# Optimization experiments

Hardware: AMD Instinct MI355X
Metric: run time of the kernel (lower is better)

Reference implementation:

```python
import jax, jax.numpy as jnp
import numpy as np

N, E, F, H, O, B = 100000, 1200000, 64, 1024, 1, 256


def _gcn_conv(x, W, b, src, dst, ew, num_nodes):
    # PyG GCNConv: out_i = sum_{(s->i)} d_i^{-1/2} w_e d_s^{-1/2} (x_s W) + b
    deg = jax.ops.segment_sum(ew, dst, num_segments=num_nodes)
    dinv = jnp.where(deg > 0, jax.lax.rsqrt(jnp.maximum(deg, 1e-12)), 0.0)
    norm = dinv[src] * ew * dinv[dst]          # [E]
    h = x @ W                                   # [N, out]
    msg = h[src] * norm[:, None]                # gather + scale
    return jax.ops.segment_sum(msg, dst, num_segments=num_nodes) + b


def setup_inputs() -> dict:
    key = jax.random.key(0)
    ks = jax.random.split(key, 12)
    def lin(k, fan_in, fan_out):
        s = 1.0 / np.sqrt(fan_in)
        kw, kb = jax.random.split(k)
        return (jax.random.uniform(kw, (fan_in, fan_out), jnp.float32, -s, s),
                jax.random.uniform(kb, (fan_out,), jnp.float32, -s, s))
    W1, b1 = lin(ks[0], F, F)
    W2, b2 = lin(ks[1], F, 2 * F)
    W3, b3 = lin(ks[2], 2 * F, 4 * F)
    Wf1, bf1 = lin(ks[3], 5 * F, H)
    Wf2, bf2 = lin(ks[4], H, O)
    feature = jax.random.normal(ks[5], (N, F), jnp.float32)
    edge_index = jax.random.randint(ks[6], (2, E), 0, N, jnp.int32)
    weight = jax.random.uniform(ks[7], (E,), jnp.float32)
    protein_batch = jnp.sort(jax.random.randint(ks[8], (N,), 0, B, jnp.int32))
    return {"feature": feature, "edge_index": edge_index, "weight": weight,
            "protein_batch": protein_batch,
            "W1": W1, "b1": b1, "W2": W2, "b2": b2, "W3": W3, "b3": b3,
            "Wf1": Wf1, "bf1": bf1, "Wf2": Wf2, "bf2": bf2}


def reference(feature, edge_index, weight, protein_batch,
              W1, b1, W2, b2, W3, b3, Wf1, bf1, Wf2, bf2):
    num_nodes = feature.shape[0]
    # add self-loops with weight 1 (PyG default)
    loop = jnp.arange(num_nodes, dtype=edge_index.dtype)
    src = jnp.concatenate([edge_index[0], loop])
    dst = jnp.concatenate([edge_index[1], loop])
    ew = jnp.concatenate([weight, jnp.ones((num_nodes,), weight.dtype)])

    x = jax.nn.relu(_gcn_conv(feature, W1, b1, src, dst, ew, num_nodes))
    x = jax.nn.relu(_gcn_conv(x, W2, b2, src, dst, ew, num_nodes))
    x = jax.nn.relu(_gcn_conv(x, W3, b3, src, dst, ew, num_nodes))
    x = jnp.concatenate([x, feature], axis=1)   # [N, 5F]

    # global_mean_pool over graph ids
    sums = jax.ops.segment_sum(x, protein_batch, num_segments=B)
    cnts = jax.ops.segment_sum(jnp.ones((num_nodes,), x.dtype), protein_batch, num_segments=B)
    gc = sums / jnp.maximum(cnts, 1.0)[:, None]

    gc = jax.nn.relu(gc @ Wf1 + bf1)            # dropout is identity in eval
    return gc @ Wf2 + bf2
```

## Files before the change

kernel.cpp:

```cpp
#include <hip/hip_runtime.h>
#include <cstdio>
#include <cstdint>

typedef _Float16 f16x8 __attribute__((ext_vector_type(8)));
typedef float f32x4 __attribute__((ext_vector_type(4)));

__device__ inline unsigned short f2bf(float f) {
  unsigned u = __float_as_uint(f);
  u += 0x7fffu + ((u >> 16) & 1u);
  return (unsigned short)(u >> 16);
}
__device__ inline float bf2f(unsigned short h) {
  return __uint_as_float(((unsigned)h) << 16);
}
__device__ inline unsigned short f2h(float f) {
  union { _Float16 h; unsigned short u; } cv;
  cv.h = (_Float16)f;
  return cv.u;
}


__global__ __launch_bounds__(256)
void k_prep(float* __restrict__ psum,
            const float* __restrict__ feature, ushort* __restrict__ featb,
            const float* __restrict__ W1, ushort* __restrict__ w1h,
            const float* __restrict__ W2, ushort* __restrict__ w2h,
            const float* __restrict__ W3, ushort* __restrict__ w3h,
            int BC, int NF, int F, int D2, int D3,
            int nB, int nC) {
  int b = blockIdx.x;
  int t = threadIdx.x;
  if (b < nB) {
    int i = b * 256 + t;
    if (i < BC) psum[i] = 0.f;
  } else if (b < nB + nC) {
    int base = ((b - nB) * 256 + t) * 4;
    if (base < NF) {
      float4 v = *reinterpret_cast<const float4*>(feature + base);
      ushort4 h;
      h.x = f2bf(v.x); h.y = f2bf(v.y); h.z = f2bf(v.z); h.w = f2bf(v.w);
      *reinterpret_cast<ushort4*>(featb + base) = h;
    }
  } else {
    int idx = (b - nB - nC) * 256 + t;
    int s1 = F * F, s2 = s1 + F * D2, s3 = s2 + D2 * D3;
    if (idx < s1) {
      int k = idx / F, n = idx - k * F;
      w1h[(size_t)n * F + k] = f2h(W1[idx]);
    } else if (idx < s2) {
      int i2 = idx - s1; int k = i2 / D2, n = i2 - k * D2;
      w2h[(size_t)n * F + k] = f2h(W2[i2]);
    } else if (idx < s3) {
      int i3 = idx - s2; int k = i3 / D3, n = i3 - k * D3;
      w3h[(size_t)n * D2 + k] = f2h(W3[i3]);
    }
  }
}

__global__ __launch_bounds__(256)
void k_gbound(const int* __restrict__ pb, int* __restrict__ gs, int N, int B) {
  int b = blockIdx.x * 256 + threadIdx.x;
  if (b > B) return;
  int lo = 0, hi = N;
  while (lo < hi) {
    int mid = (lo + hi) >> 1;
    if (pb[mid] < b) lo = mid + 1; else hi = mid;
  }
  gs[b] = lo;
}


#define EPB 4096

__global__ __launch_bounds__(256)
void k_bhist(const int* __restrict__ dst, int* __restrict__ H,
             int NB, int E) {
  __shared__ int hist[512];
  const int t = threadIdx.x;
  for (int i = t; i < NB; i += 256) hist[i] = 0;
  __syncthreads();
  const int base = blockIdx.x * EPB + t;
#pragma unroll
  for (int j = 0; j < EPB / 256; j++) {
    int e = base + 256 * j;
    if (e < E) atomicAdd(&hist[dst[e] >> 8], 1);
  }
  __syncthreads();
  for (int i = t; i < NB; i += 256) H[(size_t)blockIdx.x * NB + i] = hist[i];
}

__global__ __launch_bounds__(256)
void k_bscan1(const int* __restrict__ H, int* __restrict__ S,
              int* __restrict__ bsum, int NB, int NBLK, int T) {
  __shared__ int sh[256];
  const int t = threadIdx.x;
  const int base = blockIdx.x * 1024;
  int v[4]; int s = 0;
#pragma unroll
  for (int j = 0; j < 4; j++) {
    int idx = base + t * 4 + j;
    if (idx < T) {
      int bin = idx / NBLK, bi = idx - bin * NBLK;
      v[j] = H[(size_t)bi * NB + bin];
    } else v[j] = 0;
    s += v[j];
  }
  sh[t] = s;
  __syncthreads();
  for (int off = 1; off < 256; off <<= 1) {
    int x = (t >= off) ? sh[t - off] : 0;
    __syncthreads();
    sh[t] += x;
    __syncthreads();
  }
  int run = sh[t] - s;
#pragma unroll
  for (int j = 0; j < 4; j++) {
    int idx = base + t * 4 + j;
    if (idx < T) S[idx] = run;
    run += v[j];
  }
  if (t == 255) bsum[blockIdx.x] = sh[255];
}

__global__ __launch_bounds__(256)
void k_bscan23(int* __restrict__ S, const int* __restrict__ bsum, int T) {
  __shared__ int spre;
  const int chunk = blockIdx.x >> 2;
  if (threadIdx.x == 0) {
    int pre = 0;
    for (int t = 0; t < chunk; t++) pre += bsum[t];
    spre = pre;
  }
  __syncthreads();
  int i = blockIdx.x * 256 + threadIdx.x;
  if (i < T) S[i] += spre;
}

__global__ __launch_bounds__(256)
void k_bscatter(const int* __restrict__ src, const int* __restrict__ dst,
                const float* __restrict__ ew, const int* __restrict__ S,
                int* __restrict__ sdst, int2* __restrict__ ssw,
                int NB, int NBLK, int E) {
  __shared__ int cnt[512];
  __shared__ int sbase[512];
  const int t = threadIdx.x, bi = blockIdx.x;
  for (int i = t; i < NB; i += 256) {
    cnt[i] = 0;
    sbase[i] = S[(size_t)i * NBLK + bi];
  }
  __syncthreads();
  const int base = bi * EPB + t;
#pragma unroll
  for (int j = 0; j < EPB / 256; j++) {
    int e = base + 256 * j;
    if (e < E) {
      int d = dst[e];
      int bin = d >> 8;
      int r = atomicAdd(&cnt[bin], 1);
      int pos = sbase[bin] + r;
      sdst[pos] = d;
      ssw[pos] = make_int2(src[e], __float_as_int(ew[e]));
    }
  }
}

__global__ __launch_bounds__(256)
void k_bprocA(const int* __restrict__ sdst, const int2* __restrict__ ssw,
              const int* __restrict__ S, int* __restrict__ cntN,
              float* __restrict__ wsumN, int NB, int NBLK, int N, int E) {
  __shared__ int cnt[256];
  __shared__ float wsm[256];
  const int t = threadIdx.x, bin = blockIdx.x;
  cnt[t] = 0; wsm[t] = 0.f;
  __syncthreads();
  const int start = S[(size_t)bin * NBLK];
  const int end = (bin + 1 < NB) ? S[(size_t)(bin + 1) * NBLK] : E;
  for (int p = start + t; p < end; p += 256) {
    int ld = sdst[p] & 255;
    atomicAdd(&cnt[ld], 1);
    atomicAdd(&wsm[ld], __int_as_float(ssw[p].y));
  }
  __syncthreads();
  int n = bin * 256 + t;
  if (n < N) { cntN[n] = cnt[t]; wsumN[n] = wsm[t]; }
}

__global__ __launch_bounds__(256)
void k_scan1(const int* __restrict__ cntN, const float* __restrict__ wsumN,
             int* __restrict__ rs, int* __restrict__ bsum,
             float* __restrict__ dinv, float* __restrict__ sn, int N) {
  __shared__ int sh[256];
  const int t = threadIdx.x;
  const int base = blockIdx.x * 1024;
  int v[4]; int s = 0;
#pragma unroll
  for (int j = 0; j < 4; j++) {
    int idx = base + t * 4 + j;
    if (idx < N) {
      v[j] = cntN[idx];
      double deg = 1.0 + (double)wsumN[idx];
      float r = (float)(1.0 / sqrt(deg));
      dinv[idx] = r;
      sn[idx] = r * r;
    } else v[j] = 0;
    s += v[j];
  }
  sh[t] = s;
  __syncthreads();
  for (int off = 1; off < 256; off <<= 1) {
    int x = (t >= off) ? sh[t - off] : 0;
    __syncthreads();
    sh[t] += x;
    __syncthreads();
  }
  int run = sh[t] - s;
#pragma unroll
  for (int j = 0; j < 4; j++) {
    int idx = base + t * 4 + j;
    if (idx < N) rs[idx] = run;
    run += v[j];
  }
  if (t == 255) bsum[blockIdx.x] = sh[255];
}

__global__ __launch_bounds__(256)
void k_scan23(int* __restrict__ rs, const int* __restrict__ bsum, int N, int E) {
  __shared__ int spre;
  const int chunk = blockIdx.x >> 2;
  if (threadIdx.x == 0) {
    int pre = 0;
    for (int t = 0; t < chunk; t++) pre += bsum[t];
    spre = pre;
  }
  __syncthreads();
  int i = blockIdx.x * 256 + threadIdx.x;
  if (i < N) rs[i] += spre;
  if (i == 0) rs[N] = E;
}

__global__ __launch_bounds__(256)
void k_bprocB(const int* __restrict__ sdst, const int2* __restrict__ ssw,
              const int* __restrict__ S, const int* __restrict__ rs,
              const float* __restrict__ dinv,
              int2* __restrict__ epack, int NB, int NBLK, int N, int E) {
  __shared__ int cnt[256];
  __shared__ float sdv[256];
  __shared__ int srs[256];
  const int t = threadIdx.x, bin = blockIdx.x;
  cnt[t] = 0;
  int n = bin * 256 + t;
  sdv[t] = (n < N) ? dinv[n] : 0.f;
  srs[t] = (n < N) ? rs[n] : 0;
  __syncthreads();
  const int start = S[(size_t)bin * NBLK];
  const int end = (bin + 1 < NB) ? S[(size_t)(bin + 1) * NBLK] : E;
  for (int p = start + t; p < end; p += 256) {
    int d = sdst[p];
    int ld = d & 255;
    int2 sw = ssw[p];
    int r = atomicAdd(&cnt[ld], 1);
    float w = dinv[sw.x] * __int_as_float(sw.y) * sdv[ld];
    epack[srs[ld] + r] = make_int2(sw.x, __float_as_int(w));
  }
}


__device__ inline void bf8_fma(const int4 v, float w, float* acc) {
  acc[0] = fmaf(__uint_as_float((unsigned)v.x << 16), w, acc[0]);
  acc[1] = fmaf(__uint_as_float((unsigned)v.x & 0xffff0000u), w, acc[1]);
  acc[2] = fmaf(__uint_as_float((unsigned)v.y << 16), w, acc[2]);
  acc[3] = fmaf(__uint_as_float((unsigned)v.y & 0xffff0000u), w, acc[3]);
  acc[4] = fmaf(__uint_as_float((unsigned)v.z << 16), w, acc[4]);
  acc[5] = fmaf(__uint_as_float((unsigned)v.z & 0xffff0000u), w, acc[5]);
  acc[6] = fmaf(__uint_as_float((unsigned)v.w << 16), w, acc[6]);
  acc[7] = fmaf(__uint_as_float((unsigned)v.w & 0xffff0000u), w, acc[7]);
}

template<int LOG2L>
__global__ __launch_bounds__(256)
void k_aggregate_b(const ushort* __restrict__ Xb, const int* __restrict__ rs,
                   const int2* __restrict__ epack, const float* __restrict__ sn,
                   ushort* __restrict__ AH, int N) {
  const int t = blockIdx.x * blockDim.x + threadIdx.x;
  const int row = t >> LOG2L;
  if (row >= N) return;
  const int L = 1 << LOG2L;
  const int D = L << 3;
  const int c = (t & (L - 1)) << 3;
  const ushort* __restrict__ Xc = Xb + c;

  float acc[8];
  {
    int4 v = *reinterpret_cast<const int4*>(Xc + (size_t)row * D);
    float s = sn[row];
    acc[0] = s * __uint_as_float((unsigned)v.x << 16);
    acc[1] = s * __uint_as_float((unsigned)v.x & 0xffff0000u);
    acc[2] = s * __uint_as_float((unsigned)v.y << 16);
    acc[3] = s * __uint_as_float((unsigned)v.y & 0xffff0000u);
    acc[4] = s * __uint_as_float((unsigned)v.z << 16);
    acc[5] = s * __uint_as_float((unsigned)v.z & 0xffff0000u);
    acc[6] = s * __uint_as_float((unsigned)v.w << 16);
    acc[7] = s * __uint_as_float((unsigned)v.w & 0xffff0000u);
  }
  const int p0 = rs[row], pe = rs[row + 1];
  int i = p0;
  if ((i & 1) && i < pe) {
    int2 e = epack[i];
    int4 v = *reinterpret_cast<const int4*>(Xc + (size_t)e.x * D);
    bf8_fma(v, __int_as_float(e.y), acc);
    i++;
  }
  for (; i + 8 <= pe; i += 8) {
    int4 ea = *reinterpret_cast<const int4*>(&epack[i]);
    int4 eb = *reinterpret_cast<const int4*>(&epack[i + 2]);
    int4 ec = *reinterpret_cast<const int4*>(&epack[i + 4]);
    int4 ed = *reinterpret_cast<const int4*>(&epack[i + 6]);
    int4 v0 = *reinterpret_cast<const int4*>(Xc + (size_t)ea.x * D);
    int4 v1 = *reinterpret_cast<const int4*>(Xc + (size_t)ea.z * D);
    int4 v2 = *reinterpret_cast<const int4*>(Xc + (size_t)eb.x * D);
    int4 v3 = *reinterpret_cast<const int4*>(Xc + (size_t)eb.z * D);
    int4 v4 = *reinterpret_cast<const int4*>(Xc + (size_t)ec.x * D);
    int4 v5 = *reinterpret_cast<const int4*>(Xc + (size_t)ec.z * D);
    int4 v6 = *reinterpret_cast<const int4*>(Xc + (size_t)ed.x * D);
    int4 v7 = *reinterpret_cast<const int4*>(Xc + (size_t)ed.z * D);
    bf8_fma(v0, __int_as_float(ea.y), acc);
    bf8_fma(v1, __int_as_float(ea.w), acc);
    bf8_fma(v2, __int_as_float(eb.y), acc);
    bf8_fma(v3, __int_as_float(eb.w), acc);
    bf8_fma(v4, __int_as_float(ec.y), acc);
    bf8_fma(v5, __int_as_float(ec.w), acc);
    bf8_fma(v6, __int_as_float(ed.y), acc);
    bf8_fma(v7, __int_as_float(ed.w), acc);
  }
  if (i + 4 <= pe) {
    int4 ea = *reinterpret_cast<const int4*>(&epack[i]);
    int4 eb = *reinterpret_cast<const int4*>(&epack[i + 2]);
    int4 v0 = *reinterpret_cast<const int4*>(Xc + (size_t)ea.x * D);
    int4 v1 = *reinterpret_cast<const int4*>(Xc + (size_t)ea.z * D);
    int4 v2 = *reinterpret_cast<const int4*>(Xc + (size_t)eb.x * D);
    int4 v3 = *reinterpret_cast<const int4*>(Xc + (size_t)eb.z * D);
    bf8_fma(v0, __int_as_float(ea.y), acc);
    bf8_fma(v1, __int_as_float(ea.w), acc);
    bf8_fma(v2, __int_as_float(eb.y), acc);
    bf8_fma(v3, __int_as_float(eb.w), acc);
    i += 4;
  }
  if (i + 2 <= pe) {
    int4 e2 = *reinterpret_cast<const int4*>(&epack[i]);
    int4 v0 = *reinterpret_cast<const int4*>(Xc + (size_t)e2.x * D);
    int4 v1 = *reinterpret_cast<const int4*>(Xc + (size_t)e2.z * D);
    bf8_fma(v0, __int_as_float(e2.y), acc);
    bf8_fma(v1, __int_as_float(e2.w), acc);
    i += 2;
  }
  if (i < pe) {
    int2 e = epack[i];
    int4 v = *reinterpret_cast<const int4*>(Xc + (size_t)e.x * D);
    bf8_fma(v, __int_as_float(e.y), acc);
  }
  ushort h[8];
#pragma unroll
  for (int j = 0; j < 8; j++) h[j] = f2h(acc[j]);
  size_t o = (size_t)row * D + c;
  *reinterpret_cast<ushort4*>(AH + o)     = make_ushort4(h[0], h[1], h[2], h[3]);
  *reinterpret_cast<ushort4*>(AH + o + 4) = make_ushort4(h[4], h[5], h[6], h[7]);
}


template<int KT, int NT>
__global__ __launch_bounds__(256)
void k_gemm_mfma(const ushort* __restrict__ Ah, const ushort* __restrict__ Bh,
                 const float* __restrict__ bias, ushort* __restrict__ Y,
                 int N, int D) {
  const int t = threadIdx.x;
  const int wave = t >> 6, lane = t & 63;
  const int quad = lane >> 4, l16 = lane & 15;
  const int m0 = blockIdx.y * 128;
  const int n0 = blockIdx.x * NT;

  int r0 = m0 + wave * 32 + l16;
  int r1 = r0 + 16;
  if (r0 >= N) r0 = N - 1;
  if (r1 >= N) r1 = N - 1;
  const ushort* __restrict__ A0 = Ah + (size_t)r0 * KT;
  const ushort* __restrict__ A1 = Ah + (size_t)r1 * KT;
  const ushort* __restrict__ Bq = Bh + (size_t)(n0 + l16) * KT + quad * 8;

  f32x4 acc[2][NT / 16];
#pragma unroll
  for (int mi = 0; mi < 2; mi++)
#pragma unroll
    for (int ni = 0; ni < NT / 16; ni++) acc[mi][ni] = (f32x4){0.f, 0.f, 0.f, 0.f};

#pragma unroll
  for (int k0 = 0; k0 < KT; k0 += 32) {
    const int kk = k0 + quad * 8;
    f16x8 a0 = *reinterpret_cast<const f16x8*>(A0 + kk);
    f16x8 a1 = *reinterpret_cast<const f16x8*>(A1 + kk);
#pragma unroll
    for (int ni = 0; ni < NT / 16; ni++) {
      f16x8 bH = *reinterpret_cast<const f16x8*>(Bq + (size_t)(ni * 16) * KT + k0);
      acc[0][ni] = __builtin_amdgcn_mfma_f32_16x16x32_f16(a0, bH, acc[0][ni], 0, 0, 0);
      acc[1][ni] = __builtin_amdgcn_mfma_f32_16x16x32_f16(a1, bH, acc[1][ni], 0, 0, 0);
    }
  }

#pragma unroll
  for (int mi = 0; mi < 2; mi++) {
    int rb = m0 + wave * 32 + mi * 16 + quad * 4;
#pragma unroll
    for (int ni = 0; ni < NT / 16; ni++) {
      int col = n0 + ni * 16 + l16;
      float bv = bias[col];
#pragma unroll
      for (int r = 0; r < 4; r++) {
        int row = rb + r;
        if (row < N)
          Y[(size_t)row * D + col] = f2bf(fmaxf(acc[mi][ni][r] + bv, 0.f));
      }
    }
  }
}


#define PSPLIT 4

__global__ void k_pool(const ushort* __restrict__ X3b, const float* __restrict__ feat,
                       const int* __restrict__ gs, float* __restrict__ psum,
                       int D3, int F) {
  const int c = threadIdx.x;
  const int C = D3 + F;
  const int b = blockIdx.y;
  const int sp = blockIdx.x;
  const int s0 = gs[b], e0 = gs[b + 1];
  const int len = e0 - s0;
  if (len <= 0) return;
  const int chunk = (len + PSPLIT - 1) / PSPLIT;
  const int s = s0 + sp * chunk;
  int e = s + chunk; if (e > e0) e = e0;
  if (s >= e) return;
  const int n = e - s;
  float a0 = 0.f, a1 = 0.f, a2 = 0.f, a3 = 0.f;
  float a4 = 0.f, a5 = 0.f, a6 = 0.f, a7 = 0.f;
  if (c < D3) {
    const ushort* p = X3b + (size_t)s * D3 + c;
    int i = 0;
    for (; i + 8 <= n; i += 8) {
      a0 += bf2f(p[0 * (size_t)D3]);
      a1 += bf2f(p[1 * (size_t)D3]);
      a2 += bf2f(p[2 * (size_t)D3]);
      a3 += bf2f(p[3 * (size_t)D3]);
      a4 += bf2f(p[4 * (size_t)D3]);
      a5 += bf2f(p[5 * (size_t)D3]);
      a6 += bf2f(p[6 * (size_t)D3]);
      a7 += bf2f(p[7 * (size_t)D3]);
      p += 8 * (size_t)D3;
    }
    for (; i < n; i++) { a0 += bf2f(*p); p += D3; }
  } else {
    const float* p = feat + (size_t)s * F + (c - D3);
    int i = 0;
    for (; i + 8 <= n; i += 8) {
      a0 += p[0 * (size_t)F];
      a1 += p[1 * (size_t)F];
      a2 += p[2 * (size_t)F];
      a3 += p[3 * (size_t)F];
      a4 += p[4 * (size_t)F];
      a5 += p[5 * (size_t)F];
      a6 += p[6 * (size_t)F];
      a7 += p[7 * (size_t)F];
      p += 8 * (size_t)F;
    }
    for (; i < n; i++) { a0 += *p; p += F; }
  }
  float tot = ((a0 + a1) + (a2 + a3)) + ((a4 + a5) + (a6 + a7));
  atomicAdd(&psum[(size_t)b * C + c], tot);
}


__global__ __launch_bounds__(256)
void k_fc1(const float* __restrict__ psum, const int* __restrict__ gs,
           const float* __restrict__ Wf1, const float* __restrict__ bf1,
           float* __restrict__ hidden, int C, int Hh) {
  const int b = blockIdx.y;
  __shared__ float gcs[384];
  float invc = 1.f / fmaxf((float)(gs[b + 1] - gs[b]), 1.f);
  for (int c = threadIdx.x; c < C; c += 256)
    gcs[c] = psum[(size_t)b * C + c] * invc;
  __syncthreads();
  const int j = blockIdx.x * 256 + threadIdx.x;
  if (j >= Hh) return;
  const float* w = Wf1 + j;
  float a0 = 0.f, a1 = 0.f, a2 = 0.f, a3 = 0.f;
  int c = 0;
  for (; c + 4 <= C; c += 4) {
    a0 = fmaf(gcs[c + 0], w[(size_t)(c + 0) * Hh], a0);
    a1 = fmaf(gcs[c + 1], w[(size_t)(c + 1) * Hh], a1);
    a2 = fmaf(gcs[c + 2], w[(size_t)(c + 2) * Hh], a2);
    a3 = fmaf(gcs[c + 3], w[(size_t)(c + 3) * Hh], a3);
  }
  for (; c < C; c++) a0 = fmaf(gcs[c], w[(size_t)c * Hh], a0);
  float r = ((a0 + a1) + (a2 + a3)) + bf1[j];
  hidden[(size_t)b * Hh + j] = fmaxf(r, 0.f);
}

__global__ void k_fc2(const float* __restrict__ hidden, const float* __restrict__ Wf2,
                      const float* __restrict__ bf2, float* __restrict__ out, int Hh) {
  int b = blockIdx.x;
  int lane = threadIdx.x;
  double s = 0.0;
  for (int j = lane; j < Hh; j += 64) s += (double)hidden[(size_t)b * Hh + j] * (double)Wf2[j];
#pragma unroll
  for (int off = 32; off > 0; off >>= 1) s += __shfl_down(s, off);
  if (lane == 0) out[b] = (float)s + bf2[0];
}


extern "C" void kernel_launch(void* const* d_in, const int* in_sizes, int n_in,
                              void* d_out, int out_size, void* d_ws, size_t ws_size,
                              hipStream_t stream) {
  const float* feature = (const float*)d_in[0];
  const int*   eidx    = (const int*)  d_in[1];
  const float* weight  = (const float*)d_in[2];
  const int*   pb      = (const int*)  d_in[3];
  const float* W1  = (const float*)d_in[4];
  const float* b1  = (const float*)d_in[5];
  const float* W2  = (const float*)d_in[6];
  const float* b2  = (const float*)d_in[7];
  const float* W3  = (const float*)d_in[8];
  const float* b3  = (const float*)d_in[9];
  const float* Wf1 = (const float*)d_in[10];
  const float* bf1 = (const float*)d_in[11];
  const float* Wf2 = (const float*)d_in[12];
  const float* bf2 = (const float*)d_in[13];

  const int F  = in_sizes[5];
  const int D2 = in_sizes[7];
  const int D3 = in_sizes[9];
  const int Hh = in_sizes[11];
  const int N  = in_sizes[0] / F;
  const int E  = in_sizes[1] / 2;
  const int B  = out_size;
  const int C  = D3 + F;

  const int* srcp = eidx;
  const int* dstp = eidx + E;

  const int NB   = (N + 255) / 256;
  const int NBLK = (E + EPB - 1) / EPB;
  const int T    = NB * NBLK;
  const int nscanb = (T + 1023) / 1024;
  const int nscan  = (N + 1023) / 1024;

  auto al = [](size_t x) { return (x + 255) & ~(size_t)255; };
  size_t off = 0;
  auto alloc = [&](size_t bytes) { size_t o = off; off += al(bytes); return o; };
  size_t o_H     = alloc((size_t)T * 4);
  size_t o_S     = alloc((size_t)T * 4);
  size_t o_bsb   = alloc((size_t)nscanb * 4);
  size_t o_sdst  = alloc((size_t)E * 4);
  size_t o_ssw   = alloc((size_t)E * 8);
  size_t o_cntN  = alloc((size_t)N * 4);
  size_t o_wsumN = alloc((size_t)N * 4);
  size_t o_dinv  = alloc((size_t)N * 4);
  size_t o_sn    = alloc((size_t)N * 4);
  size_t o_rs    = alloc((size_t)(N + 1) * 4);
  size_t o_bsum  = alloc((size_t)nscan * 4);
  size_t o_epack = alloc((size_t)E * 8);
  size_t o_featb = alloc((size_t)N * F  * 2);
  size_t o_x1b   = alloc((size_t)N * F  * 2);
  size_t o_x2b   = alloc((size_t)N * D2 * 2);
  size_t o_x3b   = alloc((size_t)N * D3 * 2);
  size_t o_aggh  = alloc((size_t)N * D2 * 2);
  size_t o_w1h   = alloc((size_t)F  * F  * 2);
  size_t o_w2h   = alloc((size_t)F  * D2 * 2);
  size_t o_w3h   = alloc((size_t)D2 * D3 * 2);
  size_t o_psum  = alloc((size_t)B * C * 4);
  size_t o_gs    = alloc((size_t)(B + 1) * 4);
  size_t o_hid   = alloc((size_t)B * Hh * 4);
  if (off > ws_size) {
    fprintf(stderr, "kernel_launch: workspace too small: need %zu, have %zu\n", off, ws_size);
    return;
  }

  char* ws = (char*)d_ws;
  int*    H     = (int*)  (ws + o_H);
  int*    S     = (int*)  (ws + o_S);
  int*    bsb   = (int*)  (ws + o_bsb);
  int*    sdst  = (int*)  (ws + o_sdst);
  int2*   ssw   = (int2*) (ws + o_ssw);
  int*    cntN  = (int*)  (ws + o_cntN);
  float*  wsumN = (float*)(ws + o_wsumN);
  float*  dinv  = (float*)(ws + o_dinv);
  float*  sn    = (float*)(ws + o_sn);
  int*    rs    = (int*)  (ws + o_rs);
  int*    bsum  = (int*)  (ws + o_bsum);
  int2*   epack = (int2*) (ws + o_epack);
  ushort* featb = (ushort*)(ws + o_featb);
  ushort* x1b   = (ushort*)(ws + o_x1b);
  ushort* x2b   = (ushort*)(ws + o_x2b);
  ushort* x3b   = (ushort*)(ws + o_x3b);
  ushort* aggh  = (ushort*)(ws + o_aggh);
  ushort* w1h   = (ushort*)(ws + o_w1h);
  ushort* w2h   = (ushort*)(ws + o_w2h);
  ushort* w3h   = (ushort*)(ws + o_w3h);
  float*  psum  = (float*) (ws + o_psum);
  int*    gs    = (int*)  (ws + o_gs);
  float*  hid   = (float*)(ws + o_hid);
  float*  out   = (float*)d_out;

  const int BC = B * C, NF = N * F;
  const int nB = (BC + 255) / 256;
  const int nC = (NF / 4 + 255) / 256;
  const int nD = (F * F + F * D2 + D2 * D3 + 255) / 256;
  k_prep<<<nB + nC + nD, 256, 0, stream>>>(
      psum, feature, featb, W1, w1h, W2, w2h, W3, w3h,
      BC, NF, F, D2, D3, nB, nC);
  k_gbound<<<(B + 256) / 256, 256, 0, stream>>>(pb, gs, N, B);

  k_bhist   <<<NBLK, 256, 0, stream>>>(dstp, H, NB, E);
  k_bscan1  <<<nscanb, 256, 0, stream>>>(H, S, bsb, NB, NBLK, T);
  k_bscan23 <<<(T + 255) / 256, 256, 0, stream>>>(S, bsb, T);
  k_bscatter<<<NBLK, 256, 0, stream>>>(srcp, dstp, weight, S, sdst, ssw, NB, NBLK, E);
  k_bprocA  <<<NB, 256, 0, stream>>>(sdst, ssw, S, cntN, wsumN, NB, NBLK, N, E);
  k_scan1   <<<nscan, 256, 0, stream>>>(cntN, wsumN, rs, bsum, dinv, sn, N);
  k_scan23  <<<(N + 255) / 256, 256, 0, stream>>>(rs, bsum, N, E);
  k_bprocB  <<<NB, 256, 0, stream>>>(sdst, ssw, S, rs, dinv, epack, NB, NBLK, N, E);

  const int gy = (N + 127) / 128;

  {
    int tot = N * (F / 8);
    k_aggregate_b<3><<<(tot + 255) / 256, 256, 0, stream>>>(featb, rs, epack, sn, aggh, N);
    dim3 g(1, gy);
    k_gemm_mfma<64, 64><<<g, 256, 0, stream>>>(aggh, w1h, b1, x1b, N, F);
  }
  {
    int tot = N * (F / 8);
    k_aggregate_b<3><<<(tot + 255) / 256, 256, 0, stream>>>(x1b, rs, epack, sn, aggh, N);
    dim3 g(1, gy);
    k_gemm_mfma<64, 128><<<g, 256, 0, stream>>>(aggh, w2h, b2, x2b, N, D2);
  }
  {
    int tot = N * (D2 / 8);
    k_aggregate_b<4><<<(tot + 255) / 256, 256, 0, stream>>>(x2b, rs, epack, sn, aggh, N);
    dim3 g(2, gy);
    k_gemm_mfma<128, 128><<<g, 256, 0, stream>>>(aggh, w3h, b3, x3b, N, D3);
  }

  {
    dim3 g(PSPLIT, B);
    k_pool<<<g, C, 0, stream>>>(x3b, feature, gs, psum, D3, F);
  }
  {
    dim3 g((Hh + 255) / 256, B);
    k_fc1<<<g, 256, 0, stream>>>(psum, gs, Wf1, bf1, hid, C, Hh);
  }
  k_fc2  <<<B, 64, 0, stream>>>(hid, Wf2, bf2, out, Hh);
}
```

Baseline: 431.8 us.

## Keep weight fragments in registers and loop multiple row tiles per GEMM block

Replaces the MFMA GEMM with a variant that fixes the column tile at 64, loads all B (weight) fragments and bias into registers once, then iterates over several 128-row tiles per block. The grid for layers two and three now splits columns across more blocks and packs 2 or 4 row tiles per block. A fragments are prefetched for the full K before the MFMAs. This is meant to remove repeated weight loads per tile and cut register pressure from the wide column tiles, with launch bounds set for three blocks per CU. The trade-off is fewer blocks overall, each doing serial tile loops, and A rows are read once per column block.

```diff
diff --git a/kernel.cpp b/kernel.cpp
--- a/kernel.cpp
+++ b/kernel.cpp
@@ -368,56 +368,74 @@
 }
 
 
-template<int KT, int NT>
-__global__ __launch_bounds__(256)
-void k_gemm_mfma(const ushort* __restrict__ Ah, const ushort* __restrict__ Bh,
-                 const float* __restrict__ bias, ushort* __restrict__ Y,
-                 int N, int D) {
+template<int KT, int TPB>
+__global__ __launch_bounds__(256, 3)
+void k_gemm_rb(const ushort* __restrict__ Ah, const ushort* __restrict__ Bh,
+               const float* __restrict__ bias, ushort* __restrict__ Y,
+               int N, int D) {
+  constexpr int NT = 64;
+  constexpr int NK = KT / 32;
   const int t = threadIdx.x;
   const int wave = t >> 6, lane = t & 63;
   const int quad = lane >> 4, l16 = lane & 15;
-  const int m0 = blockIdx.y * 128;
   const int n0 = blockIdx.x * NT;
-
-  int r0 = m0 + wave * 32 + l16;
-  int r1 = r0 + 16;
-  if (r0 >= N) r0 = N - 1;
-  if (r1 >= N) r1 = N - 1;
-  const ushort* __restrict__ A0 = Ah + (size_t)r0 * KT;
-  const ushort* __restrict__ A1 = Ah + (size_t)r1 * KT;
-  const ushort* __restrict__ Bq = Bh + (size_t)(n0 + l16) * KT + quad * 8;
-
-  f32x4 acc[2][NT / 16];
-#pragma unroll
-  for (int mi = 0; mi < 2; mi++)
-#pragma unroll
-    for (int ni = 0; ni < NT / 16; ni++) acc[mi][ni] = (f32x4){0.f, 0.f, 0.f, 0.f};
-
-#pragma unroll
-  for (int k0 = 0; k0 < KT; k0 += 32) {
-    const int kk = k0 + quad * 8;
-    f16x8 a0 = *reinterpret_cast<const f16x8*>(A0 + kk);
-    f16x8 a1 = *reinterpret_cast<const f16x8*>(A1 + kk);
-#pragma unroll
-    for (int ni = 0; ni < NT / 16; ni++) {
-      f16x8 bH = *reinterpret_cast<const f16x8*>(Bq + (size_t)(ni * 16) * KT + k0);
-      acc[0][ni] = __builtin_amdgcn_mfma_f32_16x16x32_f16(a0, bH, acc[0][ni], 0, 0, 0);
-      acc[1][ni] = __builtin_amdgcn_mfma_f32_16x16x32_f16(a1, bH, acc[1][ni], 0, 0, 0);
+  const int mbase = blockIdx.y * (TPB * 128);
+
+  f16x8 bf[NK][4];
+#pragma unroll
+  for (int k0 = 0; k0 < NK; k0++)
+#pragma unroll
+    for (int ni = 0; ni < 4; ni++)
+      bf[k0][ni] = *reinterpret_cast<const f16x8*>(
+          Bh + (size_t)(n0 + ni * 16 + l16) * KT + k0 * 32 + quad * 8);
+
+  float bv[4];
+#pragma unroll
+  for (int ni = 0; ni < 4; ni++) bv[ni] = bias[n0 + ni * 16 + l16];
+
+#pragma unroll 1
+  for (int tile = 0; tile < TPB; tile++) {
+    const int rt = mbase + tile * 128 + wave * 32 + l16;
+    if (mbase + tile * 128 >= N) break;
+    int r0 = rt;      if (r0 >= N) r0 = N - 1;
+    int r1 = rt + 16; if (r1 >= N) r1 = N - 1;
+    const ushort* __restrict__ A0 = Ah + (size_t)r0 * KT + quad * 8;
+    const ushort* __restrict__ A1 = Ah + (size_t)r1 * KT + quad * 8;
+
+    f16x8 a0[NK], a1[NK];
+#pragma unroll
+    for (int k0 = 0; k0 < NK; k0++) {
+      a0[k0] = *reinterpret_cast<const f16x8*>(A0 + k0 * 32);
+      a1[k0] = *reinterpret_cast<const f16x8*>(A1 + k0 * 32);
     }
-  }
-
-#pragma unroll
-  for (int mi = 0; mi < 2; mi++) {
-    int rb = m0 + wave * 32 + mi * 16 + quad * 4;
-#pragma unroll
-    for (int ni = 0; ni < NT / 16; ni++) {
-      int col = n0 + ni * 16 + l16;
-      float bv = bias[col];
-#pragma unroll
-      for (int r = 0; r < 4; r++) {
-        int row = rb + r;
-        if (row < N)
-          Y[(size_t)row * D + col] = f2bf(fmaxf(acc[mi][ni][r] + bv, 0.f));
+
+    f32x4 acc[2][4];
+#pragma unroll
+    for (int mi = 0; mi < 2; mi++)
+#pragma unroll
+      for (int ni = 0; ni < 4; ni++) acc[mi][ni] = (f32x4){0.f, 0.f, 0.f, 0.f};
+
+#pragma unroll
+    for (int k0 = 0; k0 < NK; k0++)
+#pragma unroll
+      for (int ni = 0; ni < 4; ni++) {
+        acc[0][ni] = __builtin_amdgcn_mfma_f32_16x16x32_f16(a0[k0], bf[k0][ni], acc[0][ni], 0, 0, 0);
+        acc[1][ni] = __builtin_amdgcn_mfma_f32_16x16x32_f16(a1[k0], bf[k0][ni], acc[1][ni], 0, 0, 0);
+      }
+
+    const int rb0 = mbase + tile * 128 + wave * 32 + quad * 4;
+#pragma unroll
+    for (int mi = 0; mi < 2; mi++) {
+      int rb = rb0 + mi * 16;
+#pragma unroll
+      for (int ni = 0; ni < 4; ni++) {
+        int col = n0 + ni * 16 + l16;
+#pragma unroll
+        for (int r = 0; r < 4; r++) {
+          int row = rb + r;
+          if (row < N)
+            Y[(size_t)row * D + col] = f2bf(fmaxf(acc[mi][ni][r] + bv[ni], 0.f));
+        }
       }
     }
   }
@@ -628,25 +646,25 @@
   k_scan23  <<<(N + 255) / 256, 256, 0, stream>>>(rs, bsum, N, E);
   k_bprocB  <<<NB, 256, 0, stream>>>(sdst, ssw, S, rs, dinv, epack, NB, NBLK, N, E);
 
-  const int gy = (N + 127) / 128;
+  const int Mt = (N + 127) / 128;
 
   {
     int tot = N * (F / 8);
     k_aggregate_b<3><<<(tot + 255) / 256, 256, 0, stream>>>(featb, rs, epack, sn, aggh, N);
-    dim3 g(1, gy);
-    k_gemm_mfma<64, 64><<<g, 256, 0, stream>>>(aggh, w1h, b1, x1b, N, F);
+    dim3 g(1, Mt);
+    k_gemm_rb<64, 1><<<g, 256, 0, stream>>>(aggh, w1h, b1, x1b, N, F);
   }
   {
     int tot = N * (F / 8);
     k_aggregate_b<3><<<(tot + 255) / 256, 256, 0, stream>>>(x1b, rs, epack, sn, aggh, N);
-    dim3 g(1, gy);
-    k_gemm_mfma<64, 128><<<g, 256, 0, stream>>>(aggh, w2h, b2, x2b, N, D2);
+    dim3 g(2, (Mt + 1) / 2);
+    k_gemm_rb<64, 2><<<g, 256, 0, stream>>>(aggh, w2h, b2, x2b, N, D2);
   }
   {
     int tot = N * (D2 / 8);
     k_aggregate_b<4><<<(tot + 255) / 256, 256, 0, stream>>>(x2b, rs, epack, sn, aggh, N);
-    dim3 g(2, gy);
-    k_gemm_mfma<128, 128><<<g, 256, 0, stream>>>(aggh, w3h, b3, x3b, N, D3);
+    dim3 g(4, (Mt + 3) / 4);
+    k_gemm_rb<128, 4><<<g, 256, 0, stream>>>(aggh, w3h, b3, x3b, N, D3);
   }
 
   {
```

Result: faster. 401.8 us (-7.0%).
